# Performance work log

Hardware: AMD Instinct MI355X
Metric: run time of the kernel (lower is better)

Reference implementation:

```python
import jax, jax.numpy as jnp
import numpy as np

N_NODES = 50000


def _gine(x, src, dst, edge_embed, lin_w, lin_b, nn_w, nn_b):
    # PyG GINEConv (eps=0): out = nn(x + sum_{j->i} ReLU(x_j + lin(edge_attr)))
    e = edge_embed @ lin_w + lin_b              # [E, d_in]
    msg = jax.nn.relu(x[src] + e)               # gather + fuse, [E, d_in]
    agg = jax.ops.segment_sum(msg, dst, num_segments=N_NODES)  # scatter-add, [N, d_in]
    return (x + agg) @ nn_w + nn_b              # small MLP, [N, d_out]


def setup_inputs() -> dict:
    key = jax.random.key(0)
    ks = jax.random.split(key, 20)
    E = 800000
    h = 128
    sc = lambda f_in: 1.0 / np.sqrt(f_in)
    inp = {
        "x": jax.random.normal(ks[0], (N_NODES, 1), jnp.float32),
        "edge_index": jax.random.randint(ks[1], (2, E), 0, N_NODES, jnp.int64),
        "edge_attr": jax.random.normal(ks[2], (E, 1), jnp.float32),
        "em_w": jax.random.normal(ks[3], (1, h), jnp.float32) * sc(1),
        "em_b": jnp.zeros((h,), jnp.float32),
        "l1_w": jax.random.normal(ks[4], (h, 1), jnp.float32) * sc(h),
        "l1_b": jnp.zeros((1,), jnp.float32),
        "n1_w": jax.random.normal(ks[5], (1, h), jnp.float32) * sc(1),
        "n1_b": jnp.zeros((h,), jnp.float32),
        "l2_w": jax.random.normal(ks[6], (h, h), jnp.float32) * sc(h),
        "l2_b": jnp.zeros((h,), jnp.float32),
        "n2_w": jax.random.normal(ks[7], (h, h), jnp.float32) * sc(h),
        "n2_b": jnp.zeros((h,), jnp.float32),
        "l3_w": jax.random.normal(ks[8], (h, h), jnp.float32) * sc(h),
        "l3_b": jnp.zeros((h,), jnp.float32),
        "n3_w": jax.random.normal(ks[9], (h, h), jnp.float32) * sc(h),
        "n3_b": jnp.zeros((h,), jnp.float32),
        "dec_w": jax.random.normal(ks[10], (2 * h, 1), jnp.float32) * sc(2 * h),
        "dec_b": jnp.zeros((1,), jnp.float32),
    }
    return inp


def reference(x, edge_index, edge_attr, em_w, em_b, l1_w, l1_b, n1_w, n1_b,
              l2_w, l2_b, n2_w, n2_b, l3_w, l3_b, n3_w, n3_b, dec_w, dec_b):
    src, dst = edge_index[0], edge_index[1]
    edge_embed = edge_attr @ em_w + em_b                      # [E, 128]
    hdn = _gine(x,   src, dst, edge_embed, l1_w, l1_b, n1_w, n1_b)
    hdn = _gine(hdn, src, dst, edge_embed, l2_w, l2_b, n2_w, n2_b)
    hdn = _gine(hdn, src, dst, edge_embed, l3_w, l3_b, n3_w, n3_b)
    h_cat = jnp.concatenate([hdn[src], hdn[dst]], axis=-1)    # [E, 256]
    return h_cat @ dec_w + dec_b                              # [E, 1]
```

## Files before the change

### kernel.cpp

```cpp
#include <hip/hip_runtime.h>

#define H 128
#define CAPC 3072


typedef unsigned long long ull;
using bf16x8 = __attribute__((ext_vector_type(8))) short;
using f32x4  = __attribute__((ext_vector_type(4))) float;

__device__ int g_cursor[512];

__device__ __forceinline__ float bf2f(unsigned short v) {
  return __uint_as_float(((unsigned)v) << 16);
}
__device__ __forceinline__ unsigned short bf16r(float v) {
  unsigned u = __float_as_uint(v);
  u = (u + 0x7FFFu + ((u >> 16) & 1u)) >> 16;
  return (unsigned short)u;
}
__device__ __forceinline__ int rfl(int v) {
  return __builtin_amdgcn_readfirstlane(v);
}

__global__ __launch_bounds__(1024) void init_bin(
    const int* __restrict__ src, const int* __restrict__ dst,
    const float* __restrict__ ea,
    const float* __restrict__ em_w, const float* __restrict__ em_b,
    const float* __restrict__ l1_w, const float* __restrict__ l1_b,
    const float* __restrict__ l2_w, const float* __restrict__ l2_b,
    const float* __restrict__ n1_b,
    const float* __restrict__ l3_w, const float* __restrict__ l3_b,
    const float* __restrict__ n2w, const float* __restrict__ n3w,
    const float* __restrict__ n3b, const float* __restrict__ dec_w,
    float* __restrict__ consts, unsigned short* __restrict__ w2t,
    ull* __restrict__ spc, int E, int NBUCK) {
  const int bid = blockIdx.x;
  const int tid = threadIdx.x;
  if (bid == 0) {
    __shared__ float sa[H], sc[H];
    const int k = tid;
    if (k < H) {
      float u2 = 0.f, c2 = 0.f, u3 = 0.f, c3 = 0.f, vA = 0.f, vB = 0.f;
      for (int j = 0; j < H; ++j) {
        const float ew = em_w[j], eb = em_b[j];
        u2 = fmaf(ew, l2_w[j * H + k], u2);
        c2 = fmaf(eb, l2_w[j * H + k], c2);
        u3 = fmaf(ew, l3_w[j * H + k], u3);
        c3 = fmaf(eb, l3_w[j * H + k], c3);
        vA = fmaf(n3w[k * H + j], dec_w[j], vA);
        vB = fmaf(n3w[k * H + j], dec_w[H + j], vB);
      }
      consts[2 + k]         = u2;
      consts[2 + H + k]     = c2 + l2_b[k] + n1_b[k];
      consts[2 + 2 * H + k] = u3;
      consts[2 + 3 * H + k] = c3 + l3_b[k];
      consts[514 + k]       = vA;
      consts[642 + k]       = vB;
      sa[k] = em_w[k] * l1_w[k];
      sc[k] = em_b[k] * l1_w[k];
    }
    __syncthreads();
    for (int s = 64; s > 0; s >>= 1) {
      if (k < s) { sa[k] += sa[k + s]; sc[k] += sc[k + s]; }
      __syncthreads();
    }
    if (k == 0) { consts[0] = sa[0]; consts[1] = sc[0] + l1_b[0]; }
    __syncthreads();
    if (k < H) {
      sa[k] = n3b[k] * dec_w[k];
      sc[k] = n3b[k] * dec_w[H + k];
    }
    __syncthreads();
    for (int s = 64; s > 0; s >>= 1) {
      if (k < s) { sa[k] += sa[k + s]; sc[k] += sc[k + s]; }
      __syncthreads();
    }
    if (k == 0) { consts[770] = sa[0]; consts[771] = sc[0]; }
    return;
  }
  if (bid <= 16) {
    const int i = (bid - 1) * 1024 + tid;
    const int j = i >> 7, k = i & (H - 1);
    w2t[k * H + j] = bf16r(n2w[i]);
    return;
  }
  __shared__ int lhist[512];
  __shared__ int lbase[512];
  const int base = (bid - 17) * 2048 + tid * 2;
  if (tid < 512) lhist[tid] = 0;
  __syncthreads();
  int s_[2], d_[2], b_[2], r_[2];
  float a_[2];
#pragma unroll
  for (int j = 0; j < 2; ++j) {
    const int e = base + j;
    if (e < E) {
      s_[j] = src[e]; d_[j] = dst[e]; a_[j] = ea[e];
      b_[j] = d_[j] >> 7;
      r_[j] = atomicAdd(&lhist[b_[j]], 1);
    } else {
      b_[j] = -1;
    }
  }
  __syncthreads();
  if (tid < NBUCK && lhist[tid] > 0)
    lbase[tid] = atomicAdd(&g_cursor[tid], lhist[tid]);
  __syncthreads();
#pragma unroll
  for (int j = 0; j < 2; ++j) {
    if (b_[j] >= 0) {
      const int pl = lbase[b_[j]] + r_[j];
      if (pl < CAPC)
        spc[(size_t)b_[j] * CAPC + pl] =
            ((ull)(unsigned)(s_[j] | ((d_[j] & 127) << 16)) << 32) |
            (ull)(unsigned)__float_as_uint(a_[j]);
    }
  }
}

__global__ __launch_bounds__(1024) void fine_scatter(
    const ull* __restrict__ spc, const float* __restrict__ x,
    const float* __restrict__ consts, int2* __restrict__ spf,
    int* __restrict__ rowstart, float* __restrict__ s1, int N) {
  __shared__ int lh[128];
  __shared__ int sd[128];
  __shared__ int cur[128];
  __shared__ int2 pay[CAPC];
  const int tid = threadIdx.x;
  const int b = blockIdx.x;
  const int cnt = min(g_cursor[b], CAPC);
  const size_t rbase = (size_t)b * CAPC;
  if (tid < 128) lh[tid] = 0;
  __syncthreads();
  for (int i = tid; i < cnt; i += 1024)
    atomicAdd(&lh[(int)((spc[rbase + i] >> 48) & 127u)], 1);
  __syncthreads();
  if (tid < 128) sd[tid] = lh[tid];
  __syncthreads();
  for (int off = 1; off < 128; off <<= 1) {
    int t = 0;
    if (tid < 128 && tid >= off) t = sd[tid - off];
    __syncthreads();
    if (tid < 128) sd[tid] += t;
    __syncthreads();
  }
  if (tid < 128) {
    const int ex = sd[tid] - lh[tid];
    cur[tid] = ex;
    rowstart[b * 129 + tid] = (int)rbase + ex;
    if (tid == 0) rowstart[b * 129 + 128] = (int)rbase + cnt;
  }
  __syncthreads();
  for (int i = tid; i < cnt; i += 1024) {
    const ull payv = spc[rbase + i];
    const int dl = (int)((payv >> 48) & 127u);
    const int pos = atomicAdd(&cur[dl], 1);
    pay[pos] = make_int2((int)((payv >> 32) & 0xFFFFu), (int)(unsigned)payv);
  }
  __syncthreads();
  for (int i = tid; i < cnt; i += 1024) spf[rbase + i] = pay[i];
  const int lane = tid & 63, w = tid >> 6;
  const float a1 = consts[0], c1 = consts[1];
  for (int i = w; i < 128; i += 16) {
    const int n = (b << 7) + i;
    if (n >= N) break;
    const int rsl = sd[i] - lh[i], ci = lh[i];
    float part = 0.f;
    for (int j = lane; j < ci; j += 64) {
      const int2 pv = pay[rsl + j];
      part += fmaxf(x[pv.x] + fmaf(a1, __int_as_float(pv.y), c1), 0.f);
    }
#pragma unroll
    for (int o = 32; o >= 1; o >>= 1) part += __shfl_xor(part, o, 64);
    if (lane == 0) s1[n] = x[n] + part;
  }
}

__global__ __launch_bounds__(1024) void layer2_fused(
    const int* __restrict__ rowstart, const int2* __restrict__ sp,
    const float* __restrict__ s1, const float* __restrict__ n1w,
    const float* __restrict__ n1b, const float* __restrict__ consts,
    const unsigned short* __restrict__ w2t, const float* __restrict__ n2b,
    unsigned short* __restrict__ h2b, int N) {
  __shared__ unsigned short t2s[16][136];
  __shared__ unsigned short hs[16][128];
  const int tid = threadIdx.x, w = tid >> 6, lane = tid & 63;
  const int node0 = blockIdx.x * 16;
  {
    const int n = rfl(node0 + w);
    if (n < N) {
      const int rb = (n >> 7) * 129 + (n & 127);
      const int rs = rfl(rowstart[rb]), re = rfl(rowstart[rb + 1]);
      const float w0 = n1w[lane],             w1 = n1w[lane + 64];
      const float u0 = consts[2 + lane],      u1 = consts[2 + lane + 64];
      const float cc0 = consts[2 + H + lane], cc1 = consts[2 + H + lane + 64];
      float acc0 = 0.f, acc1 = 0.f, acc2 = 0.f, acc3 = 0.f;
      auto proc4 = [&](const int2 e0, const int2 e1, const int2 e2,
                       const int2 e3) {
        const int x0 = rfl(e0.x), x1 = rfl(e1.x), x2 = rfl(e2.x),
                  x3 = rfl(e3.x);
        const float a0 = __int_as_float(rfl(e0.y));
        const float a1 = __int_as_float(rfl(e1.y));
        const float a2 = __int_as_float(rfl(e2.y));
        const float a3 = __int_as_float(rfl(e3.y));
        const float v0 = s1[x0], v1 = s1[x1], v2 = s1[x2], v3 = s1[x3];
        acc0 += fmaxf(fmaf(v0, w0, fmaf(a0, u0, cc0)), 0.f);
        acc1 += fmaxf(fmaf(v0, w1, fmaf(a0, u1, cc1)), 0.f);
        acc2 += fmaxf(fmaf(v1, w0, fmaf(a1, u0, cc0)), 0.f);
        acc3 += fmaxf(fmaf(v1, w1, fmaf(a1, u1, cc1)), 0.f);
        acc0 += fmaxf(fmaf(v2, w0, fmaf(a2, u0, cc0)), 0.f);
        acc1 += fmaxf(fmaf(v2, w1, fmaf(a2, u1, cc1)), 0.f);
        acc2 += fmaxf(fmaf(v3, w0, fmaf(a3, u0, cc0)), 0.f);
        acc3 += fmaxf(fmaf(v3, w1, fmaf(a3, u1, cc1)), 0.f);
      };
      int j = rs;
      if (re - rs >= 4) {
        int2 e0 = sp[j], e1 = sp[j + 1], e2 = sp[j + 2], e3 = sp[j + 3];
        for (j += 4; j + 4 <= re; j += 4) {
          const int2 t0 = sp[j], t1 = sp[j + 1], t2 = sp[j + 2],
                     t3 = sp[j + 3];
          proc4(e0, e1, e2, e3);
          e0 = t0; e1 = t1; e2 = t2; e3 = t3;
        }
        proc4(e0, e1, e2, e3);
      }
      for (; j < re; ++j) {
        const int2 ev = sp[j];
        const int sx = rfl(ev.x);
        const float av = __int_as_float(rfl(ev.y));
        const float sv = s1[sx];
        acc0 += fmaxf(fmaf(sv, w0, fmaf(av, u0, cc0)), 0.f);
        acc1 += fmaxf(fmaf(sv, w1, fmaf(av, u1, cc1)), 0.f);
      }
      acc0 += acc2;
      acc1 += acc3;
      const float sn = s1[n];
      t2s[w][lane]      = bf16r(fmaf(sn, w0, n1b[lane])      + acc0);
      t2s[w][lane + 64] = bf16r(fmaf(sn, w1, n1b[lane + 64]) + acc1);
    } else {
      t2s[w][lane] = 0;
      t2s[w][lane + 64] = 0;
    }
  }
  __syncthreads();
  if (w < 8) {
    const int t = w, col = lane & 15, quad = lane >> 4;
    const bf16x8 a0 = *(const bf16x8*)&t2s[col][quad * 8];
    const bf16x8 a1 = *(const bf16x8*)&t2s[col][32 + quad * 8];
    const bf16x8 a2 = *(const bf16x8*)&t2s[col][64 + quad * 8];
    const bf16x8 a3 = *(const bf16x8*)&t2s[col][96 + quad * 8];
    const bf16x8* bcol =
        (const bf16x8*)(w2t + (size_t)(t * 16 + col) * H + quad * 8);
    f32x4 acc = {0.f, 0.f, 0.f, 0.f};
    acc = __builtin_amdgcn_mfma_f32_16x16x32_bf16(a0, bcol[0], acc, 0, 0, 0);
    acc = __builtin_amdgcn_mfma_f32_16x16x32_bf16(a1, bcol[4], acc, 0, 0, 0);
    acc = __builtin_amdgcn_mfma_f32_16x16x32_bf16(a2, bcol[8], acc, 0, 0, 0);
    acc = __builtin_amdgcn_mfma_f32_16x16x32_bf16(a3, bcol[12], acc, 0, 0, 0);
    const float bias = n2b[t * 16 + col];
#pragma unroll
    for (int r = 0; r < 4; ++r)
      hs[quad * 4 + r][t * 16 + col] = bf16r(acc[r] + bias);
  }
  __syncthreads();
  const int row = tid >> 6, word = tid & 63;
  ((unsigned*)h2b)[(size_t)(node0 + row) * 64 + word] =
      ((const unsigned*)hs)[row * 64 + word];
}

__global__ __launch_bounds__(256) void layer3_dot(
    const int* __restrict__ rowstart, const int2* __restrict__ sp,
    const unsigned short* __restrict__ h2b, const float* __restrict__ consts,
    float* __restrict__ p, float* __restrict__ q, int N) {
  const int n = rfl((blockIdx.x * blockDim.x + threadIdx.x) >> 6);
  const int lane = threadIdx.x & 63;
  if (n >= N) return;
  const int k0 = 2 * lane;
  const float u0 = consts[2 + 2 * H + k0], u1 = consts[2 + 2 * H + k0 + 1];
  const float c0 = consts[2 + 3 * H + k0], c1 = consts[2 + 3 * H + k0 + 1];
  const float vA0 = consts[514 + k0], vA1 = consts[514 + k0 + 1];
  const float vB0 = consts[642 + k0], vB1 = consts[642 + k0 + 1];
  const int rb = (n >> 7) * 129 + (n & 127);
  const int rs = rfl(rowstart[rb]), re = rfl(rowstart[rb + 1]);
  float acc0 = 0.f, acc1 = 0.f, acc2 = 0.f, acc3 = 0.f;
  auto proc8 = [&](const int2* cb) {
    int ss[8];
    float aa[8];
    ushort2 hh[8];
#pragma unroll
    for (int u = 0; u < 8; ++u) {
      ss[u] = rfl(cb[u].x);
      aa[u] = __int_as_float(rfl(cb[u].y));
    }
#pragma unroll
    for (int u = 0; u < 8; ++u)
      hh[u] = *(const ushort2*)&h2b[(size_t)ss[u] * H + k0];
#pragma unroll
    for (int u = 0; u < 8; ++u) {
      if (u & 1) {
        acc2 += fmaxf(bf2f(hh[u].x) + fmaf(aa[u], u0, c0), 0.f);
        acc3 += fmaxf(bf2f(hh[u].y) + fmaf(aa[u], u1, c1), 0.f);
      } else {
        acc0 += fmaxf(bf2f(hh[u].x) + fmaf(aa[u], u0, c0), 0.f);
        acc1 += fmaxf(bf2f(hh[u].y) + fmaf(aa[u], u1, c1), 0.f);
      }
    }
  };
  int j = rs;
  if (re - rs >= 8) {
    int2 cb[8];
#pragma unroll
    for (int u = 0; u < 8; ++u) cb[u] = sp[j + u];
    for (j += 8; j + 8 <= re; j += 8) {
      int2 tb[8];
#pragma unroll
      for (int u = 0; u < 8; ++u) tb[u] = sp[j + u];
      proc8(cb);
#pragma unroll
      for (int u = 0; u < 8; ++u) cb[u] = tb[u];
    }
    proc8(cb);
  }
  if (j + 4 <= re) {
    int ss[4];
    float aa[4];
    ushort2 hh[4];
#pragma unroll
    for (int u = 0; u < 4; ++u) {
      const int2 ev = sp[j + u];
      ss[u] = rfl(ev.x);
      aa[u] = __int_as_float(rfl(ev.y));
    }
#pragma unroll
    for (int u = 0; u < 4; ++u)
      hh[u] = *(const ushort2*)&h2b[(size_t)ss[u] * H + k0];
#pragma unroll
    for (int u = 0; u < 4; ++u) {
      acc0 += fmaxf(bf2f(hh[u].x) + fmaf(aa[u], u0, c0), 0.f);
      acc1 += fmaxf(bf2f(hh[u].y) + fmaf(aa[u], u1, c1), 0.f);
    }
    j += 4;
  }
  for (; j < re; ++j) {
    const int2 ev = sp[j];
    const int s0 = rfl(ev.x);
    const float a0 = __int_as_float(rfl(ev.y));
    const ushort2 hv = *(const ushort2*)&h2b[(size_t)s0 * H + k0];
    acc0 += fmaxf(bf2f(hv.x) + fmaf(a0, u0, c0), 0.f);
    acc1 += fmaxf(bf2f(hv.y) + fmaf(a0, u1, c1), 0.f);
  }
  acc0 += acc2;
  acc1 += acc3;
  const ushort2 hn = *(const ushort2*)&h2b[(size_t)n * H + k0];
  const float t0 = bf2f(hn.x) + acc0;
  const float t1 = bf2f(hn.y) + acc1;
  float pd = t0 * vA0 + t1 * vA1;
  float qd = t0 * vB0 + t1 * vB1;
#pragma unroll
  for (int o = 32; o >= 1; o >>= 1) {
    pd += __shfl_xor(pd, o, 64);
    qd += __shfl_xor(qd, o, 64);
  }
  if (lane == 0) {
    p[n] = pd + consts[770];
    q[n] = qd + consts[771];
  }
}

__global__ void final_kernel(const int* __restrict__ src,
                             const int* __restrict__ dst,
                             const float* __restrict__ p,
                             const float* __restrict__ q,
                             const float* __restrict__ dec_b,
                             float* __restrict__ out, int E) {
  if (blockIdx.x == 0 && threadIdx.x < 256) {
    g_cursor[threadIdx.x] = 0;
    g_cursor[threadIdx.x + 256] = 0;
  }
  const int e0 = (blockIdx.x * blockDim.x + threadIdx.x) * 2;
  if (e0 + 1 < E) {
    const int2 s2 = *(const int2*)&src[e0];
    const int2 d2 = *(const int2*)&dst[e0];
    const float db = dec_b[0];
    float2 o;
    o.x = p[s2.x] + q[d2.x] + db;
    o.y = p[s2.y] + q[d2.y] + db;
    *(float2*)&out[e0] = o;
  } else if (e0 < E) {
    out[e0] = p[src[e0]] + q[dst[e0]] + dec_b[0];
  }
}

extern "C" void kernel_launch(void* const* d_in, const int* in_sizes, int n_in,
                              void* d_out, int out_size, void* d_ws, size_t ws_size,
                              hipStream_t stream) {
  const float* x     = (const float*)d_in[0];
  const int*   ei    = (const int*)d_in[1];
  const float* ea    = (const float*)d_in[2];
  const float* em_w  = (const float*)d_in[3];
  const float* em_b  = (const float*)d_in[4];
  const float* l1_w  = (const float*)d_in[5];
  const float* l1_b  = (const float*)d_in[6];
  const float* n1_w  = (const float*)d_in[7];
  const float* n1_b  = (const float*)d_in[8];
  const float* l2_w  = (const float*)d_in[9];
  const float* l2_b  = (const float*)d_in[10];
  const float* n2_w  = (const float*)d_in[11];
  const float* n2_b  = (const float*)d_in[12];
  const float* l3_w  = (const float*)d_in[13];
  const float* l3_b  = (const float*)d_in[14];
  const float* n3_w  = (const float*)d_in[15];
  const float* n3_b  = (const float*)d_in[16];
  const float* dec_w = (const float*)d_in[17];
  const float* dec_b = (const float*)d_in[18];
  float* out = (float*)d_out;

  const int N = in_sizes[0];
  const int E = in_sizes[2];
  const int* src = ei;
  const int* dst = ei + E;

  const int NBUCK  = (N + 127) >> 7;
  const int NBATCH = (E + 2047) >> 11;
  const int NPAD   = ((N + 15) / 16) * 16;
  const int NT16   = NPAD / 16;

  float* ws       = (float*)d_ws;
  float* consts   = ws;
  ull*   spc      = (ull*)(ws + 1024);
  int2*  spf      = (int2*)(spc + (size_t)NBUCK * CAPC);
  unsigned short* h2b = (unsigned short*)(spf + (size_t)NBUCK * CAPC);
  unsigned short* w2t = h2b + (size_t)NPAD * H;
  float* s1       = (float*)(w2t + H * H);
  float* p        = s1 + N;
  float* q        = p + N;
  int*   rowstart = (int*)(q + N) + 512;

  init_bin<<<17 + NBATCH, 1024, 0, stream>>>(
      src, dst, ea, em_w, em_b, l1_w, l1_b, l2_w, l2_b, n1_b, l3_w, l3_b,
      n2_w, n3_w, n3_b, dec_w, consts, w2t, spc, E, NBUCK);
  fine_scatter<<<NBUCK, 1024, 0, stream>>>(spc, x, consts, spf, rowstart,
                                           s1, N);
  layer2_fused<<<NT16, 1024, 0, stream>>>(rowstart, spf, s1, n1_w, n1_b,
                                          consts, w2t, n2_b, h2b, N);
  layer3_dot<<<(N + 3) / 4, 256, 0, stream>>>(rowstart, spf, h2b, consts,
                                              p, q, N);
  final_kernel<<<(E / 2 + 255) / 256, 256, 0, stream>>>(src, dst, p, q, dec_b,
                                                        out, E);
}
```

Measured before the change: 208.0 us.

## Process two nodes per wave in layer2 and use wave-shuffle scan in fine_scatter

layer2_fused now runs 512 threads per block, with each wave aggregating two adjacent nodes in an interleaved loop. All 8 waves then run the MFMA stage, and the output is stored with 8-byte writes. The aim is more in-flight independent gathers per wave, which helps hide latency, and no idle waves during the MFMA. fine_scatter swaps its barrier-heavy shared-memory prefix scan for a 64-lane shuffle scan plus one cross-wave fixup, which removes many __syncthreads. The cost is higher register pressure and load imbalance when the two nodes have different degrees.

After: 209.0 us. About the same (+0.4%).

```diff
diff --git a/kernel.cpp b/kernel.cpp
--- a/kernel.cpp
+++ b/kernel.cpp
@@ -125,6 +125,7 @@
   __shared__ int lh[128];
   __shared__ int sd[128];
   __shared__ int cur[128];
+  __shared__ int sdmid;
   __shared__ int2 pay[CAPC];
   const int tid = threadIdx.x;
   const int b = blockIdx.x;
@@ -135,17 +136,18 @@
   for (int i = tid; i < cnt; i += 1024)
     atomicAdd(&lh[(int)((spc[rbase + i] >> 48) & 127u)], 1);
   __syncthreads();
-  if (tid < 128) sd[tid] = lh[tid];
-  __syncthreads();
-  for (int off = 1; off < 128; off <<= 1) {
-    int t = 0;
-    if (tid < 128 && tid >= off) t = sd[tid - off];
-    __syncthreads();
-    if (tid < 128) sd[tid] += t;
-    __syncthreads();
-  }
+  int sv = (tid < 128) ? lh[tid] : 0;
+#pragma unroll
+  for (int off = 1; off < 64; off <<= 1) {
+    const int t = __shfl_up(sv, off, 64);
+    if ((tid & 63) >= off) sv += t;
+  }
+  if (tid == 63) sdmid = sv;
+  __syncthreads();
   if (tid < 128) {
-    const int ex = sd[tid] - lh[tid];
+    if (tid >= 64) sv += sdmid;
+    sd[tid] = sv;
+    const int ex = sv - lh[tid];
     cur[tid] = ex;
     rowstart[b * 129 + tid] = (int)rbase + ex;
     if (tid == 0) rowstart[b * 129 + 128] = (int)rbase + cnt;
@@ -176,7 +178,7 @@
   }
 }
 
-__global__ __launch_bounds__(1024) void layer2_fused(
+__global__ __launch_bounds__(512) void layer2_fused(
     const int* __restrict__ rowstart, const int2* __restrict__ sp,
     const float* __restrict__ s1, const float* __restrict__ n1w,
     const float* __restrict__ n1b, const float* __restrict__ consts,
@@ -187,63 +189,118 @@
   const int tid = threadIdx.x, w = tid >> 6, lane = tid & 63;
   const int node0 = blockIdx.x * 16;
   {
-    const int n = rfl(node0 + w);
-    if (n < N) {
-      const int rb = (n >> 7) * 129 + (n & 127);
-      const int rs = rfl(rowstart[rb]), re = rfl(rowstart[rb + 1]);
-      const float w0 = n1w[lane],             w1 = n1w[lane + 64];
-      const float u0 = consts[2 + lane],      u1 = consts[2 + lane + 64];
-      const float cc0 = consts[2 + H + lane], cc1 = consts[2 + H + lane + 64];
-      float acc0 = 0.f, acc1 = 0.f, acc2 = 0.f, acc3 = 0.f;
-      auto proc4 = [&](const int2 e0, const int2 e1, const int2 e2,
-                       const int2 e3) {
-        const int x0 = rfl(e0.x), x1 = rfl(e1.x), x2 = rfl(e2.x),
-                  x3 = rfl(e3.x);
-        const float a0 = __int_as_float(rfl(e0.y));
-        const float a1 = __int_as_float(rfl(e1.y));
-        const float a2 = __int_as_float(rfl(e2.y));
-        const float a3 = __int_as_float(rfl(e3.y));
-        const float v0 = s1[x0], v1 = s1[x1], v2 = s1[x2], v3 = s1[x3];
-        acc0 += fmaxf(fmaf(v0, w0, fmaf(a0, u0, cc0)), 0.f);
-        acc1 += fmaxf(fmaf(v0, w1, fmaf(a0, u1, cc1)), 0.f);
-        acc2 += fmaxf(fmaf(v1, w0, fmaf(a1, u0, cc0)), 0.f);
-        acc3 += fmaxf(fmaf(v1, w1, fmaf(a1, u1, cc1)), 0.f);
-        acc0 += fmaxf(fmaf(v2, w0, fmaf(a2, u0, cc0)), 0.f);
-        acc1 += fmaxf(fmaf(v2, w1, fmaf(a2, u1, cc1)), 0.f);
-        acc2 += fmaxf(fmaf(v3, w0, fmaf(a3, u0, cc0)), 0.f);
-        acc3 += fmaxf(fmaf(v3, w1, fmaf(a3, u1, cc1)), 0.f);
-      };
-      int j = rs;
-      if (re - rs >= 4) {
-        int2 e0 = sp[j], e1 = sp[j + 1], e2 = sp[j + 2], e3 = sp[j + 3];
-        for (j += 4; j + 4 <= re; j += 4) {
-          const int2 t0 = sp[j], t1 = sp[j + 1], t2 = sp[j + 2],
-                     t3 = sp[j + 3];
-          proc4(e0, e1, e2, e3);
-          e0 = t0; e1 = t1; e2 = t2; e3 = t3;
-        }
-        proc4(e0, e1, e2, e3);
+    const int nA = rfl(node0 + 2 * w);
+    const int nB = nA + 1;
+    const float w0 = n1w[lane],             w1 = n1w[lane + 64];
+    const float u0 = consts[2 + lane],      u1 = consts[2 + lane + 64];
+    const float cc0 = consts[2 + H + lane], cc1 = consts[2 + H + lane + 64];
+    int rsA = 0, reA = 0, rsB = 0, reB = 0;
+    if (nA < N) {
+      const int rb = (nA >> 7) * 129 + (nA & 127);
+      rsA = rfl(rowstart[rb]);
+      reA = rfl(rowstart[rb + 1]);
+      if (nB < N) { rsB = reA; reB = rfl(rowstart[rb + 2]); }
+    }
+    float aA0 = 0.f, aA1 = 0.f, aA2 = 0.f, aA3 = 0.f;
+    float aB0 = 0.f, aB1 = 0.f, aB2 = 0.f, aB3 = 0.f;
+    auto proc4 = [&](const int2* e, float& p0, float& p1, float& p2,
+                     float& p3) {
+      const int x0 = rfl(e[0].x), x1 = rfl(e[1].x), x2 = rfl(e[2].x),
+                x3 = rfl(e[3].x);
+      const float b0 = __int_as_float(rfl(e[0].y));
+      const float b1 = __int_as_float(rfl(e[1].y));
+      const float b2 = __int_as_float(rfl(e[2].y));
+      const float b3 = __int_as_float(rfl(e[3].y));
+      const float v0 = s1[x0], v1 = s1[x1], v2 = s1[x2], v3 = s1[x3];
+      p0 += fmaxf(fmaf(v0, w0, fmaf(b0, u0, cc0)), 0.f);
+      p1 += fmaxf(fmaf(v0, w1, fmaf(b0, u1, cc1)), 0.f);
+      p2 += fmaxf(fmaf(v1, w0, fmaf(b1, u0, cc0)), 0.f);
+      p3 += fmaxf(fmaf(v1, w1, fmaf(b1, u1, cc1)), 0.f);
+      p0 += fmaxf(fmaf(v2, w0, fmaf(b2, u0, cc0)), 0.f);
+      p1 += fmaxf(fmaf(v2, w1, fmaf(b2, u1, cc1)), 0.f);
+      p2 += fmaxf(fmaf(v3, w0, fmaf(b3, u0, cc0)), 0.f);
+      p3 += fmaxf(fmaf(v3, w1, fmaf(b3, u1, cc1)), 0.f);
+    };
+    int jA = rsA, jB = rsB;
+    int2 cA[4], cB[4];
+    bool vAg = jA + 4 <= reA;
+    bool vBg = jB + 4 <= reB;
+    if (vAg) {
+#pragma unroll
+      for (int u = 0; u < 4; ++u) cA[u] = sp[jA + u];
+      jA += 4;
+    }
+    if (vBg) {
+#pragma unroll
+      for (int u = 0; u < 4; ++u) cB[u] = sp[jB + u];
+      jB += 4;
+    }
+    while (vAg || vBg) {
+      int2 tA[4], tB[4];
+      const bool nAv = vAg && (jA + 4 <= reA);
+      const bool nBv = vBg && (jB + 4 <= reB);
+      if (nAv) {
+#pragma unroll
+        for (int u = 0; u < 4; ++u) tA[u] = sp[jA + u];
       }
-      for (; j < re; ++j) {
-        const int2 ev = sp[j];
-        const int sx = rfl(ev.x);
-        const float av = __int_as_float(rfl(ev.y));
-        const float sv = s1[sx];
-        acc0 += fmaxf(fmaf(sv, w0, fmaf(av, u0, cc0)), 0.f);
-        acc1 += fmaxf(fmaf(sv, w1, fmaf(av, u1, cc1)), 0.f);
+      if (nBv) {
+#pragma unroll
+        for (int u = 0; u < 4; ++u) tB[u] = sp[jB + u];
       }
-      acc0 += acc2;
-      acc1 += acc3;
-      const float sn = s1[n];
-      t2s[w][lane]      = bf16r(fmaf(sn, w0, n1b[lane])      + acc0);
-      t2s[w][lane + 64] = bf16r(fmaf(sn, w1, n1b[lane + 64]) + acc1);
+      if (vAg) proc4(cA, aA0, aA1, aA2, aA3);
+      if (vBg) proc4(cB, aB0, aB1, aB2, aB3);
+      if (nAv) {
+#pragma unroll
+        for (int u = 0; u < 4; ++u) cA[u] = tA[u];
+        jA += 4;
+      }
+      if (nBv) {
+#pragma unroll
+        for (int u = 0; u < 4; ++u) cB[u] = tB[u];
+        jB += 4;
+      }
+      vAg = nAv;
+      vBg = nBv;
+    }
+    for (; jA < reA; ++jA) {
+      const int2 ev = sp[jA];
+      const int sx = rfl(ev.x);
+      const float av = __int_as_float(rfl(ev.y));
+      const float sv = s1[sx];
+      aA0 += fmaxf(fmaf(sv, w0, fmaf(av, u0, cc0)), 0.f);
+      aA1 += fmaxf(fmaf(sv, w1, fmaf(av, u1, cc1)), 0.f);
+    }
+    for (; jB < reB; ++jB) {
+      const int2 ev = sp[jB];
+      const int sx = rfl(ev.x);
+      const float av = __int_as_float(rfl(ev.y));
+      const float sv = s1[sx];
+      aB0 += fmaxf(fmaf(sv, w0, fmaf(av, u0, cc0)), 0.f);
+      aB1 += fmaxf(fmaf(sv, w1, fmaf(av, u1, cc1)), 0.f);
+    }
+    if (nA < N) {
+      aA0 += aA2;
+      aA1 += aA3;
+      const float sn = s1[nA];
+      t2s[2 * w][lane]      = bf16r(fmaf(sn, w0, n1b[lane])      + aA0);
+      t2s[2 * w][lane + 64] = bf16r(fmaf(sn, w1, n1b[lane + 64]) + aA1);
     } else {
-      t2s[w][lane] = 0;
-      t2s[w][lane + 64] = 0;
-    }
-  }
-  __syncthreads();
-  if (w < 8) {
+      t2s[2 * w][lane] = 0;
+      t2s[2 * w][lane + 64] = 0;
+    }
+    if (nB < N) {
+      aB0 += aB2;
+      aB1 += aB3;
+      const float sn = s1[nB];
+      t2s[2 * w + 1][lane]      = bf16r(fmaf(sn, w0, n1b[lane])      + aB0);
+      t2s[2 * w + 1][lane + 64] = bf16r(fmaf(sn, w1, n1b[lane + 64]) + aB1);
+    } else {
+      t2s[2 * w + 1][lane] = 0;
+      t2s[2 * w + 1][lane + 64] = 0;
+    }
+  }
+  __syncthreads();
+  {
     const int t = w, col = lane & 15, quad = lane >> 4;
     const bf16x8 a0 = *(const bf16x8*)&t2s[col][quad * 8];
     const bf16x8 a1 = *(const bf16x8*)&t2s[col][32 + quad * 8];
@@ -262,9 +319,9 @@
       hs[quad * 4 + r][t * 16 + col] = bf16r(acc[r] + bias);
   }
   __syncthreads();
-  const int row = tid >> 6, word = tid & 63;
-  ((unsigned*)h2b)[(size_t)(node0 + row) * 64 + word] =
-      ((const unsigned*)hs)[row * 64 + word];
+  const int row = tid >> 5, word = tid & 31;
+  ((uint2*)h2b)[(size_t)(node0 + row) * 32 + word] =
+      ((const uint2*)hs)[row * 32 + word];
 }
 
 __global__ __launch_bounds__(256) void layer3_dot(
@@ -440,8 +497,8 @@
       n2_w, n3_w, n3_b, dec_w, consts, w2t, spc, E, NBUCK);
   fine_scatter<<<NBUCK, 1024, 0, stream>>>(spc, x, consts, spf, rowstart,
                                            s1, N);
-  layer2_fused<<<NT16, 1024, 0, stream>>>(rowstart, spf, s1, n1_w, n1_b,
-                                          consts, w2t, n2_b, h2b, N);
+  layer2_fused<<<NT16, 512, 0, stream>>>(rowstart, spf, s1, n1_w, n1_b,
+                                         consts, w2t, n2_b, h2b, N);
   layer3_dot<<<(N + 3) / 4, 256, 0, stream>>>(rowstart, spf, h2b, consts,
                                               p, q, N);
   final_kernel<<<(E / 2 + 255) / 256, 256, 0, stream>>>(src, dst, p, q, dec_b,
```
